# Optimization experiments

Hardware: AMD Instinct MI355X
Metric: run time of the kernel (lower is better)

## Reference

```python
import jax, jax.numpy as jnp
import numpy as np

N_NODES = 10000
AVG_DEG = 16
N_EDGES = N_NODES * AVG_DEG
NODE_DIM, EDGE_DIM, LIN_DIM, HID, OUT, LAYERS = 9, 3, 32, 300, 2, 5


def _init(key, shape, fan_in):
    return jax.random.normal(key, shape, jnp.float32) * (1.0 / np.sqrt(fan_in))


def setup_inputs() -> dict:
    key = jax.random.key(0)
    ks = jax.random.split(key, 18)
    inp = {
        "x": jax.random.normal(ks[0], (N_NODES, NODE_DIM), jnp.float32),
        "edge_index": jax.random.randint(ks[1], (2, N_EDGES), 0, N_NODES, jnp.int32),
        "edge_attr": jax.random.normal(ks[2], (N_EDGES, EDGE_DIM), jnp.float32),
        "batch": jnp.zeros((N_NODES,), jnp.int32),
        # nn.Linear params (stored as [in, out] so fwd is x @ W + b)
        "node_w": _init(ks[3], (NODE_DIM, LIN_DIM), NODE_DIM),
        "node_b": jnp.zeros((LIN_DIM,), jnp.float32),
        "edge_w": _init(ks[4], (EDGE_DIM, LIN_DIM), EDGE_DIM),
        "edge_b": jnp.zeros((LIN_DIM,), jnp.float32),
        # GCNConv: lin (no bias) + separate additive bias (PyG convention)
        "gcn0_w": _init(ks[5], (LIN_DIM, HID), LIN_DIM),
        "gcn0_b": jnp.zeros((HID,), jnp.float32),
        "gcn_w": _init(ks[6], (LAYERS - 1, HID, HID), HID),
        "gcn_b": jnp.zeros((LAYERS - 1, HID), jnp.float32),
        "lin1_w": _init(ks[7], (HID, LIN_DIM), HID),
        "lin1_b": jnp.zeros((LIN_DIM,), jnp.float32),
        "lin2_w": _init(ks[8], (LIN_DIM, OUT), LIN_DIM),
        "lin2_b": jnp.zeros((OUT,), jnp.float32),
    }
    return inp


def reference(x, edge_index, edge_attr, batch,
              node_w, node_b, edge_w, edge_b,
              gcn0_w, gcn0_b, gcn_w, gcn_b,
              lin1_w, lin1_b, lin2_w, lin2_b):
    row, col = edge_index[0], edge_index[1]

    e = edge_attr @ edge_w + edge_b  # [E, LIN_DIM] edge embeddings

    # Faithful to the original bug: node embeddings get edge attrs scatter-added,
    # then the result is discarded by `attr = edge_attr`. Kept for fidelity (dead).
    node_h = x @ node_w + node_b
    node_h = node_h.at[row].add(e)  # unused downstream

    # GCN stack runs over the E-row edge-embedding matrix -> effective node count = E
    h = e
    n = h.shape[0]  # == N_EDGES

    # symmetric gcn_norm with self-loops (edge_weight = 1), computed once
    deg = jax.ops.segment_sum(jnp.ones((edge_index.shape[1],), h.dtype), col,
                              num_segments=n) + 1.0
    dinv = jax.lax.rsqrt(deg)
    norm = dinv[row] * dinv[col]  # per-edge normalization
    self_norm = (dinv * dinv)[:, None]  # self-loop term

    def gcn(h, w, b):
        hw = h @ w  # dense transform
        agg = jax.ops.segment_sum(hw[row] * norm[:, None], col, num_segments=n)
        return agg + self_norm * hw + b

    h = jax.nn.relu(gcn(h, gcn0_w, gcn0_b))

    def step(h, wb):
        w, b = wb
        return jax.nn.relu(gcn(h, w, b)), None

    h, _ = jax.lax.scan(step, h, (gcn_w, gcn_b))

    g = jnp.mean(h, axis=0, keepdims=True)  # [1, HID] graph readout
    g = jax.nn.relu(g @ lin1_w + lin1_b)
    pred = g @ lin2_w + lin2_b  # [1, OUT]; forward returns pre-softmax logits
    return pred
```

## Files before the change

kernel.cpp:

```cpp
#include <hip/hip_runtime.h>
#include <hip/hip_bf16.h>

#define N_NODES 10000
#define N_EDGES 160000
#define HID 300
#define HIDP 304
#define NPARTB (N_EDGES - N_NODES)
#define KS 328
#define RBM 80
#define RBF 16
#define PARTB_BLOCKS 1875
#define GEMMA_BLOCKS 125
#define FILL_BLOCKS 313
#define MEGA_BLOCKS (PARTB_BLOCKS + GEMMA_BLOCKS + FILL_BLOCKS)
#define FUSE_BLOCKS 625

typedef __attribute__((ext_vector_type(8))) short short8;
typedef __attribute__((ext_vector_type(4))) short s16x4;
typedef __attribute__((ext_vector_type(4))) float f32x4;

#define MFMA_B16(a, b, c) __builtin_amdgcn_mfma_f32_16x16x32_bf16(a, b, c, 0, 0, 0)

__device__ __forceinline__ short bf16r(float x) {
    unsigned u = __float_as_uint(x);
    return (short)((u + 0x7fffu + ((u >> 16) & 1u)) >> 16);
}
__device__ __forceinline__ float b2f(unsigned short u) {
    return __uint_as_float(((unsigned)u) << 16);
}
__device__ __forceinline__ void split1(float x, short& hi, short& lo) {
    short h = bf16r(x);
    float hf = __uint_as_float(((unsigned)(unsigned short)h) << 16);
    hi = h;
    lo = bf16r(x - hf);
}

__global__ void k_prep(const float* __restrict__ g0w, const float* __restrict__ gw,
                       short* __restrict__ wt0, short* __restrict__ wtl,
                       const int* __restrict__ col, int* __restrict__ cnt) {
    int idx = blockIdx.x * 256 + threadIdx.x;
    if (idx < N_EDGES) atomicAdd(&cnt[col[idx]], 1);
    if (idx < 1216) {
        int n16 = idx & 15, q = (idx >> 4) & 3, nt = idx >> 6;
        int n = nt * 16 + n16;
        short* hd = wt0 + (size_t)(nt * 8 + q) * 128 + n16 * 8;
        short* ld = wt0 + (size_t)(nt * 8 + 4 + q) * 128 + n16 * 8;
#pragma unroll
        for (int j = 0; j < 8; ++j) {
            int k = q * 8 + j;
            float f = (n < HID) ? g0w[k * HID + n] : 0.0f;
            short hi, lo;
            split1(f, hi, lo);
            hd[j] = hi;
            ld[j] = lo;
        }
    } else if (idx < 1216 + 48640) {
        int i = idx - 1216;
        int n16 = i & 15; i >>= 4;
        int q = i & 3; i >>= 2;
        int nt = i % 19; i /= 19;
        int chunk = i % 10;
        int l = i / 10;
        int n = nt * 16 + n16;
        int cnt_idx = chunk * 19 + nt;
        short* base = wtl + (size_t)l * 194560;
        short* hd = base + (size_t)(cnt_idx * 8 + q) * 128 + n16 * 8;
        short* ld = base + (size_t)(cnt_idx * 8 + 4 + q) * 128 + n16 * 8;
#pragma unroll
        for (int j = 0; j < 8; ++j) {
            int k = chunk * 32 + q * 8 + j;
            float f = (k < HID && n < HID) ? gw[((size_t)l * HID + k) * HID + n] : 0.0f;
            short hi, lo;
            split1(f, hi, lo);
            hd[j] = hi;
            ld[j] = lo;
        }
    }
}

__global__ __launch_bounds__(1024) void k_scan(
    const int* __restrict__ cnt, int* __restrict__ col_start,
    int* __restrict__ cursor, float* __restrict__ dinv,
    float* __restrict__ selfnorm) {
    __shared__ int wsum[16];
    int t = threadIdx.x;
    int lane = t & 63, w = t >> 6;
    int carry = 0;
    for (int base = 0; base < N_NODES; base += 1024) {
        int i = base + t;
        int v = (i < N_NODES) ? cnt[i] : 0;
        int s = v;
#pragma unroll
        for (int d = 1; d < 64; d <<= 1) {
            int n = __shfl_up(s, d, 64);
            if (lane >= d) s += n;
        }
        if (lane == 63) wsum[w] = s;
        __syncthreads();
        int woff = 0, total = 0;
#pragma unroll
        for (int k = 0; k < 16; ++k) {
            if (k < w) woff += wsum[k];
            total += wsum[k];
        }
        if (i < N_NODES) {
            int excl = carry + woff + s - v;
            col_start[i] = excl;
            cursor[i] = excl;
            float dd = (float)v + 1.0f;
            dinv[i] = rsqrtf(dd);
            selfnorm[i] = 1.0f / dd;
        }
        carry += total;
        __syncthreads();
    }
    if (t == 0) col_start[N_NODES] = carry;
}

template <int MT, int NTC>
__device__ __forceinline__ void kloop(const short* __restrict__ wp, int nch,
                                      const short* Hh, int nt0, int quad, int l16,
                                      f32x4 (&acc)[MT][NTC]) {
#pragma unroll
    for (int mt = 0; mt < MT; ++mt)
#pragma unroll
        for (int i = 0; i < NTC; ++i)
#pragma unroll
            for (int r = 0; r < 4; ++r) acc[mt][i][r] = 0.0f;

    const short* a0 = Hh + l16 * KS + quad * 8;
    const short* w0 = wp + (size_t)nt0 * 1024 + (size_t)(quad * 128 + l16 * 8);

    short8 ah[MT], an[MT], b1[NTC], b1n[NTC], b2[NTC];
#pragma unroll
    for (int mt = 0; mt < MT; ++mt) ah[mt] = *(const short8*)(a0 + mt * 16 * KS);
#pragma unroll
    for (int i = 0; i < NTC; ++i) b1[i] = *(const short8*)(w0 + (size_t)i * 1024);

#pragma unroll 1
    for (int c = 0; c < nch - 1; ++c) {
        const short* wc = w0 + (size_t)c * 19456;
        const short* wn = wc + 19456;
        const short* apn = a0 + (c + 1) * 32;
#pragma unroll
        for (int i = 0; i < NTC; ++i) b2[i] = *(const short8*)(wc + (size_t)i * 1024 + 512);
#pragma unroll
        for (int mt = 0; mt < MT; ++mt) an[mt] = *(const short8*)(apn + mt * 16 * KS);
#pragma unroll
        for (int i = 0; i < NTC; ++i) b1n[i] = *(const short8*)(wn + (size_t)i * 1024);
#pragma unroll
        for (int mt = 0; mt < MT; ++mt)
#pragma unroll
            for (int i = 0; i < NTC; ++i) acc[mt][i] = MFMA_B16(ah[mt], b1[i], acc[mt][i]);
#pragma unroll
        for (int mt = 0; mt < MT; ++mt)
#pragma unroll
            for (int i = 0; i < NTC; ++i) acc[mt][i] = MFMA_B16(ah[mt], b2[i], acc[mt][i]);
#pragma unroll
        for (int mt = 0; mt < MT; ++mt) ah[mt] = an[mt];
#pragma unroll
        for (int i = 0; i < NTC; ++i) b1[i] = b1n[i];
    }
    {
        const short* wc = w0 + (size_t)(nch - 1) * 19456;
#pragma unroll
        for (int i = 0; i < NTC; ++i) b2[i] = *(const short8*)(wc + (size_t)i * 1024 + 512);
#pragma unroll
        for (int mt = 0; mt < MT; ++mt)
#pragma unroll
            for (int i = 0; i < NTC; ++i) acc[mt][i] = MFMA_B16(ah[mt], b1[i], acc[mt][i]);
#pragma unroll
        for (int mt = 0; mt < MT; ++mt)
#pragma unroll
            for (int i = 0; i < NTC; ++i) acc[mt][i] = MFMA_B16(ah[mt], b2[i], acc[mt][i]);
    }
}

template <int MT, int NTC>
__device__ __forceinline__ void gcn_epilogue(const float* __restrict__ bias,
                                             int nt0, int quad, int l16,
                                             f32x4 (&acc)[MT][NTC], short* Hh) {
#pragma unroll
    for (int i = 0; i < NTC; ++i) {
        int c = (nt0 + i) * 16 + l16;
        float b = (c < HID) ? bias[c] : 0.0f;
#pragma unroll
        for (int mt = 0; mt < MT; ++mt)
#pragma unroll
            for (int r = 0; r < 4; ++r) {
                float v = fmaxf(acc[mt][i][r] + b, 0.0f);
                Hh[(mt * 16 + quad * 4 + r) * KS + c] = bf16r(v);
            }
    }
}

template <int MT, int NTC>
__device__ __forceinline__ void gcn_final(const float* __restrict__ bias,
                                          int nt0, int quad, int l16,
                                          f32x4 (&acc)[MT][NTC],
                                          float* __restrict__ gout) {
#pragma unroll
    for (int i = 0; i < NTC; ++i) {
        int c = (nt0 + i) * 16 + l16;
        float b = (c < HID) ? bias[c] : 0.0f;
        float s = 0.0f;
#pragma unroll
        for (int mt = 0; mt < MT; ++mt)
#pragma unroll
            for (int r = 0; r < 4; ++r) s += fmaxf(acc[mt][i][r] + b, 0.0f);
        s += __shfl_xor(s, 16, 64);
        s += __shfl_xor(s, 32, 64);
        if (quad == 0) gout[c] = (c < HID) ? s : 0.0f;
    }
}

template <int MT, int NTC>
__device__ __forceinline__ void gemm_out(int base, int nt0, int quad, int l16,
                                         f32x4 (&acc)[MT][NTC],
                                         unsigned short* __restrict__ HW) {
#pragma unroll
    for (int i = 0; i < NTC; ++i) {
        int c = (nt0 + i) * 16 + l16;
#pragma unroll
        for (int mt = 0; mt < MT; ++mt)
#pragma unroll
            for (int r = 0; r < 4; ++r) {
                int gm = base + mt * 16 + quad * 4 + r;
                if (gm < N_NODES)
                    HW[(size_t)gm * HIDP + c] = (unsigned short)bf16r(acc[mt][i][r]);
            }
    }
}

__global__ __launch_bounds__(512, 3) void k_mega(
    const float* __restrict__ edge_attr,
    const float* __restrict__ edge_w,
    const float* __restrict__ edge_b,
    const short* __restrict__ wt0,
    const short* __restrict__ wtl,
    const float* __restrict__ gcn0_b,
    const float* __restrict__ gcn_b,
    float* __restrict__ gpartB,
    unsigned short* __restrict__ hw0,
    const int* __restrict__ row,
    const int* __restrict__ col,
    int* __restrict__ cursor,
    const float* __restrict__ dinv,
    int2* __restrict__ edge_pack) {
    __shared__ short Hh[RBM * KS];
    int bid = blockIdx.x, t = threadIdx.x;
    int lane = t & 63, w = t >> 6;
    int l16 = lane & 15, quad = lane >> 4;
    int nt0 = (w < 3) ? w * 3 : 9 + (w - 3) * 2;

    if (bid < PARTB_BLOCKS) {
        int base = N_NODES + bid * RBM;
        for (int i = t; i < RBM * 8; i += 512) {
            int r = i >> 3, c4 = (i & 7) * 4;
            const float* ar = edge_attr + (size_t)(base + r) * 3;
            float a0 = ar[0], a1 = ar[1], a2 = ar[2];
#pragma unroll
            for (int j = 0; j < 4; ++j) {
                int cc = c4 + j;
                float v = edge_b[cc];
                v = fmaf(a0, edge_w[cc], v);
                v = fmaf(a1, edge_w[32 + cc], v);
                v = fmaf(a2, edge_w[64 + cc], v);
                Hh[r * KS + cc] = bf16r(v);
            }
        }
        for (int i = t; i < RBM * 24; i += 512) {
            int r = i / 24, k = 304 + i % 24;
            Hh[r * KS + k] = 0;
        }
        __syncthreads();

        float* gout = gpartB + (size_t)bid * HIDP;
        if (w < 3) {
            f32x4 acc[5][3];
            kloop<5, 3>(wt0, 1, Hh, nt0, quad, l16, acc);
            __syncthreads();
            gcn_epilogue<5, 3>(gcn0_b, nt0, quad, l16, acc, Hh);
            __syncthreads();
            for (int l = 0; l < 4; ++l) {
                kloop<5, 3>(wtl + (size_t)l * 194560, 10, Hh, nt0, quad, l16, acc);
                __syncthreads();
                if (l < 3) {
                    gcn_epilogue<5, 3>(gcn_b + l * HID, nt0, quad, l16, acc, Hh);
                    __syncthreads();
                } else {
                    gcn_final<5, 3>(gcn_b + l * HID, nt0, quad, l16, acc, gout);
                }
            }
        } else {
            f32x4 acc[5][2];
            kloop<5, 2>(wt0, 1, Hh, nt0, quad, l16, acc);
            __syncthreads();
            gcn_epilogue<5, 2>(gcn0_b, nt0, quad, l16, acc, Hh);
            __syncthreads();
            for (int l = 0; l < 4; ++l) {
                kloop<5, 2>(wtl + (size_t)l * 194560, 10, Hh, nt0, quad, l16, acc);
                __syncthreads();
                if (l < 3) {
                    gcn_epilogue<5, 2>(gcn_b + l * HID, nt0, quad, l16, acc, Hh);
                    __syncthreads();
                } else {
                    gcn_final<5, 2>(gcn_b + l * HID, nt0, quad, l16, acc, gout);
                }
            }
        }
    } else if (bid < PARTB_BLOCKS + GEMMA_BLOCKS) {
        int base = (bid - PARTB_BLOCKS) * RBM;
        for (int i = t; i < RBM * 8; i += 512) {
            int r = i >> 3, c4 = (i & 7) * 4;
            const float* ar = edge_attr + (size_t)(base + r) * 3;
            float a0 = ar[0], a1 = ar[1], a2 = ar[2];
#pragma unroll
            for (int j = 0; j < 4; ++j) {
                int cc = c4 + j;
                float v = edge_b[cc];
                v = fmaf(a0, edge_w[cc], v);
                v = fmaf(a1, edge_w[32 + cc], v);
                v = fmaf(a2, edge_w[64 + cc], v);
                Hh[r * KS + cc] = bf16r(v);
            }
        }
        for (int i = t; i < RBM * 24; i += 512) {
            int r = i / 24, k = 304 + i % 24;
            Hh[r * KS + k] = 0;
        }
        __syncthreads();
        if (w < 3) {
            f32x4 acc[5][3];
            kloop<5, 3>(wt0, 1, Hh, nt0, quad, l16, acc);
            gemm_out<5, 3>(base, nt0, quad, l16, acc, hw0);
        } else {
            f32x4 acc[5][2];
            kloop<5, 2>(wt0, 1, Hh, nt0, quad, l16, acc);
            gemm_out<5, 2>(base, nt0, quad, l16, acc, hw0);
        }
    } else {
        int e = (bid - PARTB_BLOCKS - GEMMA_BLOCKS) * 512 + t;
        if (e < N_EDGES) {
            int c = col[e], r = row[e];
            int p = atomicAdd(&cursor[c], 1);
            edge_pack[p] = make_int2(r, __float_as_int(dinv[r] * dinv[c]));
        }
    }
}

__device__ __forceinline__ void agg_row(int c, int lane,
                                        const unsigned short* __restrict__ hw_in,
                                        const int* __restrict__ col_start,
                                        const int2* __restrict__ edge_pack,
                                        float (&v)[5]) {
#pragma unroll
    for (int jj = 0; jj < 5; ++jj) v[jj] = 0.0f;
    int beg = col_start[c], end = col_start[c + 1];
    int i = beg;
#pragma unroll 1
    for (; i + 8 <= end; i += 8) {
        int2 e0 = edge_pack[i], e1 = edge_pack[i + 1];
        int2 e2 = edge_pack[i + 2], e3 = edge_pack[i + 3];
        int2 e4 = edge_pack[i + 4], e5 = edge_pack[i + 5];
        int2 e6 = edge_pack[i + 6], e7 = edge_pack[i + 7];
        const unsigned short* h0 = hw_in + (size_t)e0.x * HIDP;
        const unsigned short* h1 = hw_in + (size_t)e1.x * HIDP;
        const unsigned short* h2 = hw_in + (size_t)e2.x * HIDP;
        const unsigned short* h3 = hw_in + (size_t)e3.x * HIDP;
        const unsigned short* h4 = hw_in + (size_t)e4.x * HIDP;
        const unsigned short* h5 = hw_in + (size_t)e5.x * HIDP;
        const unsigned short* h6 = hw_in + (size_t)e6.x * HIDP;
        const unsigned short* h7 = hw_in + (size_t)e7.x * HIDP;
        float n0 = __int_as_float(e0.y), n1 = __int_as_float(e1.y);
        float n2 = __int_as_float(e2.y), n3 = __int_as_float(e3.y);
        float n4 = __int_as_float(e4.y), n5 = __int_as_float(e5.y);
        float n6 = __int_as_float(e6.y), n7 = __int_as_float(e7.y);
#pragma unroll
        for (int jj = 0; jj < 5; ++jj) {
            int cc = lane + 64 * jj;
            if (cc < HIDP) {
                float s = v[jj];
                s = fmaf(n0, b2f(h0[cc]), s);
                s = fmaf(n1, b2f(h1[cc]), s);
                s = fmaf(n2, b2f(h2[cc]), s);
                s = fmaf(n3, b2f(h3[cc]), s);
                s = fmaf(n4, b2f(h4[cc]), s);
                s = fmaf(n5, b2f(h5[cc]), s);
                s = fmaf(n6, b2f(h6[cc]), s);
                s = fmaf(n7, b2f(h7[cc]), s);
                v[jj] = s;
            }
        }
    }
#pragma unroll 1
    for (; i + 4 <= end; i += 4) {
        int2 e0 = edge_pack[i], e1 = edge_pack[i + 1];
        int2 e2 = edge_pack[i + 2], e3 = edge_pack[i + 3];
        const unsigned short* h0 = hw_in + (size_t)e0.x * HIDP;
        const unsigned short* h1 = hw_in + (size_t)e1.x * HIDP;
        const unsigned short* h2 = hw_in + (size_t)e2.x * HIDP;
        const unsigned short* h3 = hw_in + (size_t)e3.x * HIDP;
        float n0 = __int_as_float(e0.y), n1 = __int_as_float(e1.y);
        float n2 = __int_as_float(e2.y), n3 = __int_as_float(e3.y);
#pragma unroll
        for (int jj = 0; jj < 5; ++jj) {
            int cc = lane + 64 * jj;
            if (cc < HIDP) {
                float s = v[jj];
                s = fmaf(n0, b2f(h0[cc]), s);
                s = fmaf(n1, b2f(h1[cc]), s);
                s = fmaf(n2, b2f(h2[cc]), s);
                s = fmaf(n3, b2f(h3[cc]), s);
                v[jj] = s;
            }
        }
    }
#pragma unroll 1
    for (; i < end; ++i) {
        int2 e0 = edge_pack[i];
        const unsigned short* h0 = hw_in + (size_t)e0.x * HIDP;
        float n0 = __int_as_float(e0.y);
#pragma unroll
        for (int jj = 0; jj < 5; ++jj) {
            int cc = lane + 64 * jj;
            if (cc < HIDP) v[jj] = fmaf(n0, b2f(h0[cc]), v[jj]);
        }
    }
}

__global__ __launch_bounds__(512, 4) void k_fuse(
    const unsigned short* __restrict__ hw_in,
    const int* __restrict__ col_start,
    const int2* __restrict__ edge_pack,
    const float* __restrict__ selfnorm,
    const float* __restrict__ bias,
    const short* __restrict__ wt,
    unsigned short* __restrict__ hw_out) {
    __shared__ short Hh[RBF * KS];
    int t = threadIdx.x;
    int lane = t & 63, w = t >> 6;
    int l16 = lane & 15, quad = lane >> 4;
    int base = blockIdx.x * RBF;
    int nt0 = (w < 3) ? w * 3 : 9 + (w - 3) * 2;

#pragma unroll 1
    for (int j = 0; j < 2; ++j) {
        int r = w * 2 + j;
        int c = base + r;
        float v[5];
        agg_row(c, lane, hw_in, col_start, edge_pack, v);
        float sn = selfnorm[c];
        const unsigned short* sp = hw_in + (size_t)c * HIDP;
#pragma unroll
        for (int jj = 0; jj < 5; ++jj) {
            int cc = lane + 64 * jj;
            if (cc < HIDP) {
                float h = v[jj] + sn * b2f(sp[cc]) + ((cc < HID) ? bias[cc] : 0.0f);
                Hh[r * KS + cc] = bf16r(fmaxf(h, 0.0f));
            }
        }
    }
    for (int i = t; i < RBF * 6; i += 512) {
        int r = i / 6, k = 304 + (i % 6) * 4;
        *(s16x4*)&Hh[r * KS + k] = (s16x4)0;
    }
    __syncthreads();

    if (w < 3) {
        f32x4 acc[1][3];
        kloop<1, 3>(wt, 10, Hh, nt0, quad, l16, acc);
        gemm_out<1, 3>(base, nt0, quad, l16, acc, hw_out);
    } else {
        f32x4 acc[1][2];
        kloop<1, 2>(wt, 10, Hh, nt0, quad, l16, acc);
        gemm_out<1, 2>(base, nt0, quad, l16, acc, hw_out);
    }
}

__global__ __launch_bounds__(512) void k_last(
    const unsigned short* __restrict__ hw_in,
    const int* __restrict__ col_start,
    const int2* __restrict__ edge_pack,
    const float* __restrict__ selfnorm,
    const float* __restrict__ bias,
    const float* __restrict__ gpartB,
    float* __restrict__ g_sum) {
    __shared__ float red[8 * 320];
    int t = threadIdx.x;
    int lane = t & 63, w = t >> 6;
    int base = blockIdx.x * RBF;

    float s[5] = {0.0f, 0.0f, 0.0f, 0.0f, 0.0f};
#pragma unroll 1
    for (int j = 0; j < 2; ++j) {
        int c = base + w * 2 + j;
        float v[5];
        agg_row(c, lane, hw_in, col_start, edge_pack, v);
        float sn = selfnorm[c];
        const unsigned short* sp = hw_in + (size_t)c * HIDP;
#pragma unroll
        for (int jj = 0; jj < 5; ++jj) {
            int cc = lane + 64 * jj;
            if (cc < HID) {
                float h = v[jj] + sn * b2f(sp[cc]) + bias[cc];
                s[jj] += fmaxf(h, 0.0f);
            }
        }
    }
    if (w < 3) {
        int rr = blockIdx.x * 3 + w;
        if (rr < PARTB_BLOCKS) {
#pragma unroll
            for (int jj = 0; jj < 5; ++jj) {
                int cc = lane + 64 * jj;
                if (cc < HID) s[jj] += gpartB[(size_t)rr * HIDP + cc];
            }
        }
    }
#pragma unroll
    for (int jj = 0; jj < 5; ++jj) red[w * 320 + lane + 64 * jj] = s[jj];
    __syncthreads();
    if (w == 0) {
#pragma unroll
        for (int jj = 0; jj < 5; ++jj) {
            int cc = lane + 64 * jj;
            if (cc < HID) {
                float tot = 0.0f;
#pragma unroll
                for (int g = 0; g < 8; ++g) tot += red[g * 320 + cc];
                atomicAdd(&g_sum[cc], tot);
            }
        }
    }
}

__global__ void k_head(const float* __restrict__ g_sum,
                       const float* __restrict__ lin1_w, const float* __restrict__ lin1_b,
                       const float* __restrict__ lin2_w, const float* __restrict__ lin2_b,
                       float* __restrict__ out) {
    __shared__ float g2[32];
    int t = threadIdx.x;
    const float inv = 1.0f / (float)N_EDGES;
    if (t < 32) {
        float a = lin1_b[t];
        for (int d = 0; d < HID; ++d) a = fmaf(g_sum[d] * inv, lin1_w[d * 32 + t], a);
        g2[t] = fmaxf(a, 0.0f);
    }
    __syncthreads();
    if (t < 2) {
        float p = lin2_b[t];
        for (int j = 0; j < 32; ++j) p = fmaf(g2[j], lin2_w[j * 2 + t], p);
        out[t] = p;
    }
}


extern "C" void kernel_launch(void* const* d_in, const int* in_sizes, int n_in,
                              void* d_out, int out_size, void* d_ws, size_t ws_size,
                              hipStream_t stream) {
    (void)in_sizes; (void)n_in; (void)out_size; (void)ws_size;
    const int* edge_index = (const int*)d_in[1];
    const float* edge_attr = (const float*)d_in[2];
    const float* edge_w = (const float*)d_in[6];
    const float* edge_b = (const float*)d_in[7];
    const float* gcn0_w = (const float*)d_in[8];
    const float* gcn0_b = (const float*)d_in[9];
    const float* gcn_w = (const float*)d_in[10];
    const float* gcn_b = (const float*)d_in[11];
    const float* lin1_w = (const float*)d_in[12];
    const float* lin1_b = (const float*)d_in[13];
    const float* lin2_w = (const float*)d_in[14];
    const float* lin2_b = (const float*)d_in[15];

    char* ws = (char*)d_ws;
    size_t off = 0;
    auto alloc = [&](size_t bytes) {
        void* p = ws + off;
        off = (off + bytes + 255) & ~(size_t)255;
        return p;
    };
    unsigned short* hwA = (unsigned short*)alloc((size_t)N_NODES * HIDP * 2);
    unsigned short* hwB = (unsigned short*)alloc((size_t)N_NODES * HIDP * 2);
    int2* edge_pack = (int2*)alloc((size_t)N_EDGES * 8);
    int* cnt = (int*)alloc((size_t)N_NODES * 4);
    int* col_start = (int*)alloc((size_t)(N_NODES + 1) * 4);
    int* cursor = (int*)alloc((size_t)N_NODES * 4);
    float* dinv = (float*)alloc((size_t)N_NODES * 4);
    float* selfnorm = (float*)alloc((size_t)N_NODES * 4);
    float* g_sum = (float*)alloc((size_t)HIDP * 4);
    short* wt0 = (short*)alloc((size_t)38912);
    short* wtl = (short*)alloc((size_t)4 * 389120);
    float* gpartB = (float*)alloc((size_t)PARTB_BLOCKS * HIDP * 4);

    const int* row = edge_index;
    const int* col = edge_index + N_EDGES;

    hipMemsetAsync(cnt, 0, N_NODES * 4, stream);
    hipMemsetAsync(g_sum, 0, HIDP * 4, stream);

    k_prep<<<(N_EDGES + 255) / 256, 256, 0, stream>>>(gcn0_w, gcn_w, wt0, wtl, col, cnt);
    k_scan<<<1, 1024, 0, stream>>>(cnt, col_start, cursor, dinv, selfnorm);

    k_mega<<<MEGA_BLOCKS, 512, 0, stream>>>(edge_attr, edge_w, edge_b, wt0, wtl,
                                            gcn0_b, gcn_b, gpartB, hwA,
                                            row, col, cursor, dinv, edge_pack);

    k_fuse<<<FUSE_BLOCKS, 512, 0, stream>>>(hwA, col_start, edge_pack, selfnorm,
                                            gcn0_b, wtl + (size_t)0 * 194560, hwB);
    k_fuse<<<FUSE_BLOCKS, 512, 0, stream>>>(hwB, col_start, edge_pack, selfnorm,
                                            gcn_b + 0 * HID, wtl + (size_t)1 * 194560, hwA);
    k_fuse<<<FUSE_BLOCKS, 512, 0, stream>>>(hwA, col_start, edge_pack, selfnorm,
                                            gcn_b + 1 * HID, wtl + (size_t)2 * 194560, hwB);
    k_fuse<<<FUSE_BLOCKS, 512, 0, stream>>>(hwB, col_start, edge_pack, selfnorm,
                                            gcn_b + 2 * HID, wtl + (size_t)3 * 194560, hwA);
    k_last<<<FUSE_BLOCKS, 512, 0, stream>>>(hwA, col_start, edge_pack, selfnorm,
                                            gcn_b + 3 * HID, gpartB, g_sum);
    k_head<<<1, 64, 0, stream>>>(g_sum, lin1_w, lin1_b, lin2_w, lin2_b, (float*)d_out);
}
```

Baseline: 492.9 us.

## Vectorize aggregation gathers to 4-wide bf16 loads and simplify GEMM k-loop

The edge aggregation in the fused and last-layer kernels now has each lane gather 4 contiguous bf16 values per neighbor row with 8-byte loads, two chunks per lane, instead of 5 scalar 2-byte loads. This is meant to cut the number of memory instructions in the gather-bound aggregation. The MFMA k-loop drops its software-pipelined register prefetch for a simpler load-then-compute loop, which may expose more load latency but uses fewer registers. The mega kernel's launch bound rises to 4 waves per EU, trading registers for occupancy.

```diff
diff --git a/kernel.cpp b/kernel.cpp
--- a/kernel.cpp
+++ b/kernel.cpp
@@ -28,6 +28,12 @@
 __device__ __forceinline__ float b2f(unsigned short u) {
     return __uint_as_float(((unsigned)u) << 16);
 }
+__device__ __forceinline__ float blo(unsigned u) {
+    return __uint_as_float(u << 16);
+}
+__device__ __forceinline__ float bhi(unsigned u) {
+    return __uint_as_float(u & 0xffff0000u);
+}
 __device__ __forceinline__ void split1(float x, short& hi, short& lo) {
     short h = bf16r(x);
     float hf = __uint_as_float(((unsigned)(unsigned short)h) << 16);
@@ -127,52 +133,28 @@
         for (int i = 0; i < NTC; ++i)
 #pragma unroll
             for (int r = 0; r < 4; ++r) acc[mt][i][r] = 0.0f;
-
-    const short* a0 = Hh + l16 * KS + quad * 8;
-    const short* w0 = wp + (size_t)nt0 * 1024 + (size_t)(quad * 128 + l16 * 8);
-
-    short8 ah[MT], an[MT], b1[NTC], b1n[NTC], b2[NTC];
-#pragma unroll
-    for (int mt = 0; mt < MT; ++mt) ah[mt] = *(const short8*)(a0 + mt * 16 * KS);
-#pragma unroll
-    for (int i = 0; i < NTC; ++i) b1[i] = *(const short8*)(w0 + (size_t)i * 1024);
-
 #pragma unroll 1
-    for (int c = 0; c < nch - 1; ++c) {
-        const short* wc = w0 + (size_t)c * 19456;
-        const short* wn = wc + 19456;
-        const short* apn = a0 + (c + 1) * 32;
-#pragma unroll
-        for (int i = 0; i < NTC; ++i) b2[i] = *(const short8*)(wc + (size_t)i * 1024 + 512);
-#pragma unroll
-        for (int mt = 0; mt < MT; ++mt) an[mt] = *(const short8*)(apn + mt * 16 * KS);
-#pragma unroll
-        for (int i = 0; i < NTC; ++i) b1n[i] = *(const short8*)(wn + (size_t)i * 1024);
+    for (int c = 0; c < nch; ++c) {
+        const short* cb = wp + (size_t)(c * 19 + nt0) * 1024 + quad * 128 + l16 * 8;
+        short8 ah[MT];
 #pragma unroll
         for (int mt = 0; mt < MT; ++mt)
-#pragma unroll
-            for (int i = 0; i < NTC; ++i) acc[mt][i] = MFMA_B16(ah[mt], b1[i], acc[mt][i]);
+            ah[mt] = *(const short8*)&Hh[(mt * 16 + l16) * KS + c * 32 + quad * 8];
+        short8 bb[NTC];
+#pragma unroll
+        for (int i = 0; i < NTC; ++i) bb[i] = *(const short8*)(cb + (size_t)i * 1024);
 #pragma unroll
         for (int mt = 0; mt < MT; ++mt)
 #pragma unroll
-            for (int i = 0; i < NTC; ++i) acc[mt][i] = MFMA_B16(ah[mt], b2[i], acc[mt][i]);
-#pragma unroll
-        for (int mt = 0; mt < MT; ++mt) ah[mt] = an[mt];
-#pragma unroll
-        for (int i = 0; i < NTC; ++i) b1[i] = b1n[i];
-    }
-    {
-        const short* wc = w0 + (size_t)(nch - 1) * 19456;
-#pragma unroll
-        for (int i = 0; i < NTC; ++i) b2[i] = *(const short8*)(wc + (size_t)i * 1024 + 512);
+            for (int i = 0; i < NTC; ++i)
+                acc[mt][i] = MFMA_B16(ah[mt], bb[i], acc[mt][i]);
+#pragma unroll
+        for (int i = 0; i < NTC; ++i) bb[i] = *(const short8*)(cb + (size_t)i * 1024 + 512);
 #pragma unroll
         for (int mt = 0; mt < MT; ++mt)
 #pragma unroll
-            for (int i = 0; i < NTC; ++i) acc[mt][i] = MFMA_B16(ah[mt], b1[i], acc[mt][i]);
-#pragma unroll
-        for (int mt = 0; mt < MT; ++mt)
-#pragma unroll
-            for (int i = 0; i < NTC; ++i) acc[mt][i] = MFMA_B16(ah[mt], b2[i], acc[mt][i]);
+            for (int i = 0; i < NTC; ++i)
+                acc[mt][i] = MFMA_B16(ah[mt], bb[i], acc[mt][i]);
     }
 }
 
@@ -232,7 +214,7 @@
     }
 }
 
-__global__ __launch_bounds__(512, 3) void k_mega(
+__global__ __launch_bounds__(512, 4) void k_mega(
     const float* __restrict__ edge_attr,
     const float* __restrict__ edge_w,
     const float* __restrict__ edge_b,
@@ -349,14 +331,23 @@
     }
 }
 
-__device__ __forceinline__ void agg_row(int c, int lane,
-                                        const unsigned short* __restrict__ hw_in,
-                                        const int* __restrict__ col_start,
-                                        const int2* __restrict__ edge_pack,
-                                        float (&v)[5]) {
-#pragma unroll
-    for (int jj = 0; jj < 5; ++jj) v[jj] = 0.0f;
+__device__ __forceinline__ void fma4(float (&v)[4], float n, uint2 q) {
+    v[0] = fmaf(n, blo(q.x), v[0]);
+    v[1] = fmaf(n, bhi(q.x), v[1]);
+    v[2] = fmaf(n, blo(q.y), v[2]);
+    v[3] = fmaf(n, bhi(q.y), v[3]);
+}
+
+__device__ __forceinline__ void agg_row4(int c, int lane,
+                                         const unsigned short* __restrict__ hw_in,
+                                         const int* __restrict__ col_start,
+                                         const int2* __restrict__ edge_pack,
+                                         float (&v0)[4], float (&v1)[4]) {
+#pragma unroll
+    for (int k = 0; k < 4; ++k) { v0[k] = 0.0f; v1[k] = 0.0f; }
     int beg = col_start[c], end = col_start[c + 1];
+    int cb0 = 4 * lane;
+    int cb1 = 256 + 4 * lane;
     int i = beg;
 #pragma unroll 1
     for (; i + 8 <= end; i += 8) {
@@ -372,26 +363,26 @@
         const unsigned short* h5 = hw_in + (size_t)e5.x * HIDP;
         const unsigned short* h6 = hw_in + (size_t)e6.x * HIDP;
         const unsigned short* h7 = hw_in + (size_t)e7.x * HIDP;
+        uint2 a0 = *(const uint2*)(h0 + cb0), b0 = *(const uint2*)(h0 + cb1);
+        uint2 a1 = *(const uint2*)(h1 + cb0), b1 = *(const uint2*)(h1 + cb1);
+        uint2 a2 = *(const uint2*)(h2 + cb0), b2 = *(const uint2*)(h2 + cb1);
+        uint2 a3 = *(const uint2*)(h3 + cb0), b3 = *(const uint2*)(h3 + cb1);
+        uint2 a4 = *(const uint2*)(h4 + cb0), b4 = *(const uint2*)(h4 + cb1);
+        uint2 a5 = *(const uint2*)(h5 + cb0), b5 = *(const uint2*)(h5 + cb1);
+        uint2 a6 = *(const uint2*)(h6 + cb0), b6 = *(const uint2*)(h6 + cb1);
+        uint2 a7 = *(const uint2*)(h7 + cb0), b7 = *(const uint2*)(h7 + cb1);
         float n0 = __int_as_float(e0.y), n1 = __int_as_float(e1.y);
         float n2 = __int_as_float(e2.y), n3 = __int_as_float(e3.y);
         float n4 = __int_as_float(e4.y), n5 = __int_as_float(e5.y);
         float n6 = __int_as_float(e6.y), n7 = __int_as_float(e7.y);
-#pragma unroll
-        for (int jj = 0; jj < 5; ++jj) {
-            int cc = lane + 64 * jj;
-            if (cc < HIDP) {
-                float s = v[jj];
-                s = fmaf(n0, b2f(h0[cc]), s);
-                s = fmaf(n1, b2f(h1[cc]), s);
-                s = fmaf(n2, b2f(h2[cc]), s);
-                s = fmaf(n3, b2f(h3[cc]), s);
-                s = fmaf(n4, b2f(h4[cc]), s);
-                s = fmaf(n5, b2f(h5[cc]), s);
-                s = fmaf(n6, b2f(h6[cc]), s);
-                s = fmaf(n7, b2f(h7[cc]), s);
-                v[jj] = s;
-            }
-        }
+        fma4(v0, n0, a0); fma4(v1, n0, b0);
+        fma4(v0, n1, a1); fma4(v1, n1, b1);
+        fma4(v0, n2, a2); fma4(v1, n2, b2);
+        fma4(v0, n3, a3); fma4(v1, n3, b3);
+        fma4(v0, n4, a4); fma4(v1, n4, b4);
+        fma4(v0, n5, a5); fma4(v1, n5, b5);
+        fma4(v0, n6, a6); fma4(v1, n6, b6);
+        fma4(v0, n7, a7); fma4(v1, n7, b7);
     }
 #pragma unroll 1
     for (; i + 4 <= end; i += 4) {
@@ -401,31 +392,24 @@
         const unsigned short* h1 = hw_in + (size_t)e1.x * HIDP;
         const unsigned short* h2 = hw_in + (size_t)e2.x * HIDP;
         const unsigned short* h3 = hw_in + (size_t)e3.x * HIDP;
+        uint2 a0 = *(const uint2*)(h0 + cb0), b0 = *(const uint2*)(h0 + cb1);
+        uint2 a1 = *(const uint2*)(h1 + cb0), b1 = *(const uint2*)(h1 + cb1);
+        uint2 a2 = *(const uint2*)(h2 + cb0), b2 = *(const uint2*)(h2 + cb1);
+        uint2 a3 = *(const uint2*)(h3 + cb0), b3 = *(const uint2*)(h3 + cb1);
         float n0 = __int_as_float(e0.y), n1 = __int_as_float(e1.y);
         float n2 = __int_as_float(e2.y), n3 = __int_as_float(e3.y);
-#pragma unroll
-        for (int jj = 0; jj < 5; ++jj) {
-            int cc = lane + 64 * jj;
-            if (cc < HIDP) {
-                float s = v[jj];
-                s = fmaf(n0, b2f(h0[cc]), s);
-                s = fmaf(n1, b2f(h1[cc]), s);
-                s = fmaf(n2, b2f(h2[cc]), s);
-                s = fmaf(n3, b2f(h3[cc]), s);
-                v[jj] = s;
-            }
-        }
+        fma4(v0, n0, a0); fma4(v1, n0, b0);
+        fma4(v0, n1, a1); fma4(v1, n1, b1);
+        fma4(v0, n2, a2); fma4(v1, n2, b2);
+        fma4(v0, n3, a3); fma4(v1, n3, b3);
     }
 #pragma unroll 1
     for (; i < end; ++i) {
         int2 e0 = edge_pack[i];
         const unsigned short* h0 = hw_in + (size_t)e0.x * HIDP;
+        uint2 a0 = *(const uint2*)(h0 + cb0), b0 = *(const uint2*)(h0 + cb1);
         float n0 = __int_as_float(e0.y);
-#pragma unroll
-        for (int jj = 0; jj < 5; ++jj) {
-            int cc = lane + 64 * jj;
-            if (cc < HIDP) v[jj] = fmaf(n0, b2f(h0[cc]), v[jj]);
-        }
+        fma4(v0, n0, a0); fma4(v1, n0, b0);
     }
 }
 
@@ -443,22 +427,35 @@
     int l16 = lane & 15, quad = lane >> 4;
     int base = blockIdx.x * RBF;
     int nt0 = (w < 3) ? w * 3 : 9 + (w - 3) * 2;
+    int cb0 = 4 * lane, cb1 = 256 + 4 * lane;
 
 #pragma unroll 1
     for (int j = 0; j < 2; ++j) {
         int r = w * 2 + j;
         int c = base + r;
-        float v[5];
-        agg_row(c, lane, hw_in, col_start, edge_pack, v);
+        float v0[4], v1[4];
+        agg_row4(c, lane, hw_in, col_start, edge_pack, v0, v1);
         float sn = selfnorm[c];
         const unsigned short* sp = hw_in + (size_t)c * HIDP;
-#pragma unroll
-        for (int jj = 0; jj < 5; ++jj) {
-            int cc = lane + 64 * jj;
-            if (cc < HIDP) {
-                float h = v[jj] + sn * b2f(sp[cc]) + ((cc < HID) ? bias[cc] : 0.0f);
-                Hh[r * KS + cc] = bf16r(fmaxf(h, 0.0f));
-            }
+        uint2 s0 = *(const uint2*)(sp + cb0);
+        float4 bv = *(const float4*)(bias + cb0);
+        s16x4 pk;
+        pk[0] = bf16r(fmaxf(v0[0] + sn * blo(s0.x) + bv.x, 0.0f));
+        pk[1] = bf16r(fmaxf(v0[1] + sn * bhi(s0.x) + bv.y, 0.0f));
+        pk[2] = bf16r(fmaxf(v0[2] + sn * blo(s0.y) + bv.z, 0.0f));
+        pk[3] = bf16r(fmaxf(v0[3] + sn * bhi(s0.y) + bv.w, 0.0f));
+        *(s16x4*)&Hh[r * KS + cb0] = pk;
+        if (lane < 12) {
+            uint2 s1 = *(const uint2*)(sp + cb1);
+            float sv[4] = {sn * blo(s1.x), sn * bhi(s1.x), sn * blo(s1.y), sn * bhi(s1.y)};
+            s16x4 pk2;
+#pragma unroll
+            for (int k = 0; k < 4; ++k) {
+                int cc = cb1 + k;
+                float b = (cc < HID) ? bias[cc] : 0.0f;
+                pk2[k] = bf16r(fmaxf(v1[k] + sv[k] + b, 0.0f));
+            }
+            *(s16x4*)&Hh[r * KS + cb1] = pk2;
         }
     }
     for (int i = t; i < RBF * 6; i += 512) {
@@ -490,46 +487,70 @@
     int t = threadIdx.x;
     int lane = t & 63, w = t >> 6;
     int base = blockIdx.x * RBF;
-
-    float s[5] = {0.0f, 0.0f, 0.0f, 0.0f, 0.0f};
+    int cb0 = 4 * lane, cb1 = 256 + 4 * lane;
+
+    float s0[4] = {0.0f, 0.0f, 0.0f, 0.0f};
+    float s1[4] = {0.0f, 0.0f, 0.0f, 0.0f};
 #pragma unroll 1
     for (int j = 0; j < 2; ++j) {
         int c = base + w * 2 + j;
-        float v[5];
-        agg_row(c, lane, hw_in, col_start, edge_pack, v);
+        float v0[4], v1[4];
+        agg_row4(c, lane, hw_in, col_start, edge_pack, v0, v1);
         float sn = selfnorm[c];
         const unsigned short* sp = hw_in + (size_t)c * HIDP;
-#pragma unroll
-        for (int jj = 0; jj < 5; ++jj) {
-            int cc = lane + 64 * jj;
-            if (cc < HID) {
-                float h = v[jj] + sn * b2f(sp[cc]) + bias[cc];
-                s[jj] += fmaxf(h, 0.0f);
+        uint2 q0 = *(const uint2*)(sp + cb0);
+        float4 bv = *(const float4*)(bias + cb0);
+        s0[0] += fmaxf(v0[0] + sn * blo(q0.x) + bv.x, 0.0f);
+        s0[1] += fmaxf(v0[1] + sn * bhi(q0.x) + bv.y, 0.0f);
+        s0[2] += fmaxf(v0[2] + sn * blo(q0.y) + bv.z, 0.0f);
+        s0[3] += fmaxf(v0[3] + sn * bhi(q0.y) + bv.w, 0.0f);
+        if (lane < 12) {
+            uint2 q1 = *(const uint2*)(sp + cb1);
+            float sv[4] = {sn * blo(q1.x), sn * bhi(q1.x), sn * blo(q1.y), sn * bhi(q1.y)};
+#pragma unroll
+            for (int k = 0; k < 4; ++k) {
+                int cc = cb1 + k;
+                if (cc < HID) s1[k] += fmaxf(v1[k] + sv[k] + bias[cc], 0.0f);
             }
         }
     }
     if (w < 3) {
         int rr = blockIdx.x * 3 + w;
         if (rr < PARTB_BLOCKS) {
-#pragma unroll
-            for (int jj = 0; jj < 5; ++jj) {
-                int cc = lane + 64 * jj;
-                if (cc < HID) s[jj] += gpartB[(size_t)rr * HIDP + cc];
-            }
-        }
-    }
-#pragma unroll
-    for (int jj = 0; jj < 5; ++jj) red[w * 320 + lane + 64 * jj] = s[jj];
+            const float* gp = gpartB + (size_t)rr * HIDP;
+            float4 g0 = *(const float4*)(gp + cb0);
+            s0[0] += g0.x; s0[1] += g0.y; s0[2] += g0.z; s0[3] += g0.w;
+            if (lane < 12) {
+#pragma unroll
+                for (int k = 0; k < 4; ++k) {
+                    int cc = cb1 + k;
+                    if (cc < HID) s1[k] += gp[cc];
+                }
+            }
+        }
+    }
+    *(float4*)&red[w * 320 + cb0] = make_float4(s0[0], s0[1], s0[2], s0[3]);
+    if (lane < 12) *(float4*)&red[w * 320 + cb1] = make_float4(s1[0], s1[1], s1[2], s1[3]);
     __syncthreads();
     if (w == 0) {
 #pragma unroll
-        for (int jj = 0; jj < 5; ++jj) {
-            int cc = lane + 64 * jj;
-            if (cc < HID) {
-                float tot = 0.0f;
-#pragma unroll
-                for (int g = 0; g < 8; ++g) tot += red[g * 320 + cc];
-                atomicAdd(&g_sum[cc], tot);
+        for (int k = 0; k < 4; ++k) {
+            int cc = cb0 + k;
+            float tot = 0.0f;
+#pragma unroll
+            for (int g = 0; g < 8; ++g) tot += red[g * 320 + cc];
+            atomicAdd(&g_sum[cc], tot);
+        }
+        if (lane < 12) {
+#pragma unroll
+            for (int k = 0; k < 4; ++k) {
+                int cc = cb1 + k;
+                if (cc < HID) {
+                    float tot = 0.0f;
+#pragma unroll
+                    for (int g = 0; g < 8; ++g) tot += red[g * 320 + cc];
+                    atomicAdd(&g_sum[cc], tot);
+                }
             }
         }
     }
```

Result: slower. 526.6 us (+6.8%).

## Interleave two-row aggregation in fuse/last kernels and simplify mega GEMM loop

Applied to the files above, without the earlier changes.

Replaces the per-row sequential neighbor aggregation with a paired routine that gathers four edges for each of two destination rows at once, raising memory-level parallelism in the gather. The old software-pipelined k-loop is renamed kloop_p and used by k_fuse, while a simpler non-pipelined kloop is now used by k_mega. k_mega's launch bounds change from 3 to 4 waves per SIMD to raise occupancy. The simpler loop and tighter register budget may lose latency hiding or cause spills in the GEMM phase.

```diff
diff --git a/kernel.cpp b/kernel.cpp
--- a/kernel.cpp
+++ b/kernel.cpp
@@ -127,6 +127,41 @@
         for (int i = 0; i < NTC; ++i)
 #pragma unroll
             for (int r = 0; r < 4; ++r) acc[mt][i][r] = 0.0f;
+#pragma unroll 1
+    for (int c = 0; c < nch; ++c) {
+        const short* cb = wp + (size_t)(c * 19 + nt0) * 1024 + quad * 128 + l16 * 8;
+        short8 ah[MT];
+#pragma unroll
+        for (int mt = 0; mt < MT; ++mt)
+            ah[mt] = *(const short8*)&Hh[(mt * 16 + l16) * KS + c * 32 + quad * 8];
+        short8 bb[NTC];
+#pragma unroll
+        for (int i = 0; i < NTC; ++i) bb[i] = *(const short8*)(cb + (size_t)i * 1024);
+#pragma unroll
+        for (int mt = 0; mt < MT; ++mt)
+#pragma unroll
+            for (int i = 0; i < NTC; ++i)
+                acc[mt][i] = MFMA_B16(ah[mt], bb[i], acc[mt][i]);
+#pragma unroll
+        for (int i = 0; i < NTC; ++i) bb[i] = *(const short8*)(cb + (size_t)i * 1024 + 512);
+#pragma unroll
+        for (int mt = 0; mt < MT; ++mt)
+#pragma unroll
+            for (int i = 0; i < NTC; ++i)
+                acc[mt][i] = MFMA_B16(ah[mt], bb[i], acc[mt][i]);
+    }
+}
+
+template <int MT, int NTC>
+__device__ __forceinline__ void kloop_p(const short* __restrict__ wp, int nch,
+                                        const short* Hh, int nt0, int quad, int l16,
+                                        f32x4 (&acc)[MT][NTC]) {
+#pragma unroll
+    for (int mt = 0; mt < MT; ++mt)
+#pragma unroll
+        for (int i = 0; i < NTC; ++i)
+#pragma unroll
+            for (int r = 0; r < 4; ++r) acc[mt][i][r] = 0.0f;
 
     const short* a0 = Hh + l16 * KS + quad * 8;
     const short* w0 = wp + (size_t)nt0 * 1024 + (size_t)(quad * 128 + l16 * 8);
@@ -232,7 +267,7 @@
     }
 }
 
-__global__ __launch_bounds__(512, 3) void k_mega(
+__global__ __launch_bounds__(512, 4) void k_mega(
     const float* __restrict__ edge_attr,
     const float* __restrict__ edge_w,
     const float* __restrict__ edge_b,
@@ -349,82 +384,100 @@
     }
 }
 
-__device__ __forceinline__ void agg_row(int c, int lane,
-                                        const unsigned short* __restrict__ hw_in,
-                                        const int* __restrict__ col_start,
-                                        const int2* __restrict__ edge_pack,
-                                        float (&v)[5]) {
-#pragma unroll
-    for (int jj = 0; jj < 5; ++jj) v[jj] = 0.0f;
-    int beg = col_start[c], end = col_start[c + 1];
-    int i = beg;
+__device__ __forceinline__ void agg_edge4(int i, int lane, int cap,
+                                          const unsigned short* __restrict__ hw_in,
+                                          const int2* __restrict__ ep,
+                                          float (&v)[5]) {
+    int2 e0 = ep[i], e1 = ep[i + 1], e2 = ep[i + 2], e3 = ep[i + 3];
+    const unsigned short* h0 = hw_in + (size_t)e0.x * HIDP;
+    const unsigned short* h1 = hw_in + (size_t)e1.x * HIDP;
+    const unsigned short* h2 = hw_in + (size_t)e2.x * HIDP;
+    const unsigned short* h3 = hw_in + (size_t)e3.x * HIDP;
+    float n0 = __int_as_float(e0.y), n1 = __int_as_float(e1.y);
+    float n2 = __int_as_float(e2.y), n3 = __int_as_float(e3.y);
+#pragma unroll
+    for (int jj = 0; jj < 5; ++jj) {
+        int cc = lane + 64 * jj;
+        if (cc < cap) {
+            float s = v[jj];
+            s = fmaf(n0, b2f(h0[cc]), s);
+            s = fmaf(n1, b2f(h1[cc]), s);
+            s = fmaf(n2, b2f(h2[cc]), s);
+            s = fmaf(n3, b2f(h3[cc]), s);
+            v[jj] = s;
+        }
+    }
+}
+
+__device__ __forceinline__ void agg_pair(int c0, int c1, int lane,
+                                         const unsigned short* __restrict__ hw_in,
+                                         const int* __restrict__ col_start,
+                                         const int2* __restrict__ ep,
+                                         float (&v0)[5], float (&v1)[5]) {
+#pragma unroll
+    for (int jj = 0; jj < 5; ++jj) { v0[jj] = 0.0f; v1[jj] = 0.0f; }
+    int i0 = col_start[c0], e0 = col_start[c0 + 1];
+    int i1 = col_start[c1], e1 = col_start[c1 + 1];
 #pragma unroll 1
-    for (; i + 8 <= end; i += 8) {
-        int2 e0 = edge_pack[i], e1 = edge_pack[i + 1];
-        int2 e2 = edge_pack[i + 2], e3 = edge_pack[i + 3];
-        int2 e4 = edge_pack[i + 4], e5 = edge_pack[i + 5];
-        int2 e6 = edge_pack[i + 6], e7 = edge_pack[i + 7];
-        const unsigned short* h0 = hw_in + (size_t)e0.x * HIDP;
-        const unsigned short* h1 = hw_in + (size_t)e1.x * HIDP;
-        const unsigned short* h2 = hw_in + (size_t)e2.x * HIDP;
-        const unsigned short* h3 = hw_in + (size_t)e3.x * HIDP;
-        const unsigned short* h4 = hw_in + (size_t)e4.x * HIDP;
-        const unsigned short* h5 = hw_in + (size_t)e5.x * HIDP;
-        const unsigned short* h6 = hw_in + (size_t)e6.x * HIDP;
-        const unsigned short* h7 = hw_in + (size_t)e7.x * HIDP;
-        float n0 = __int_as_float(e0.y), n1 = __int_as_float(e1.y);
-        float n2 = __int_as_float(e2.y), n3 = __int_as_float(e3.y);
-        float n4 = __int_as_float(e4.y), n5 = __int_as_float(e5.y);
-        float n6 = __int_as_float(e6.y), n7 = __int_as_float(e7.y);
+    while (i0 + 4 <= e0 && i1 + 4 <= e1) {
+        int2 a0 = ep[i0], a1 = ep[i0 + 1], a2 = ep[i0 + 2], a3 = ep[i0 + 3];
+        int2 b0 = ep[i1], b1 = ep[i1 + 1], b2 = ep[i1 + 2], b3 = ep[i1 + 3];
+        const unsigned short* pa0 = hw_in + (size_t)a0.x * HIDP;
+        const unsigned short* pa1 = hw_in + (size_t)a1.x * HIDP;
+        const unsigned short* pa2 = hw_in + (size_t)a2.x * HIDP;
+        const unsigned short* pa3 = hw_in + (size_t)a3.x * HIDP;
+        const unsigned short* pb0 = hw_in + (size_t)b0.x * HIDP;
+        const unsigned short* pb1 = hw_in + (size_t)b1.x * HIDP;
+        const unsigned short* pb2 = hw_in + (size_t)b2.x * HIDP;
+        const unsigned short* pb3 = hw_in + (size_t)b3.x * HIDP;
+        float na0 = __int_as_float(a0.y), na1 = __int_as_float(a1.y);
+        float na2 = __int_as_float(a2.y), na3 = __int_as_float(a3.y);
+        float nb0 = __int_as_float(b0.y), nb1 = __int_as_float(b1.y);
+        float nb2 = __int_as_float(b2.y), nb3 = __int_as_float(b3.y);
 #pragma unroll
         for (int jj = 0; jj < 5; ++jj) {
             int cc = lane + 64 * jj;
             if (cc < HIDP) {
-                float s = v[jj];
-                s = fmaf(n0, b2f(h0[cc]), s);
-                s = fmaf(n1, b2f(h1[cc]), s);
-                s = fmaf(n2, b2f(h2[cc]), s);
-                s = fmaf(n3, b2f(h3[cc]), s);
-                s = fmaf(n4, b2f(h4[cc]), s);
-                s = fmaf(n5, b2f(h5[cc]), s);
-                s = fmaf(n6, b2f(h6[cc]), s);
-                s = fmaf(n7, b2f(h7[cc]), s);
-                v[jj] = s;
-            }
-        }
+                float s = v0[jj];
+                s = fmaf(na0, b2f(pa0[cc]), s);
+                s = fmaf(na1, b2f(pa1[cc]), s);
+                s = fmaf(na2, b2f(pa2[cc]), s);
+                s = fmaf(na3, b2f(pa3[cc]), s);
+                v0[jj] = s;
+                float u = v1[jj];
+                u = fmaf(nb0, b2f(pb0[cc]), u);
+                u = fmaf(nb1, b2f(pb1[cc]), u);
+                u = fmaf(nb2, b2f(pb2[cc]), u);
+                u = fmaf(nb3, b2f(pb3[cc]), u);
+                v1[jj] = u;
+            }
+        }
+        i0 += 4; i1 += 4;
     }
 #pragma unroll 1
-    for (; i + 4 <= end; i += 4) {
-        int2 e0 = edge_pack[i], e1 = edge_pack[i + 1];
-        int2 e2 = edge_pack[i + 2], e3 = edge_pack[i + 3];
-        const unsigned short* h0 = hw_in + (size_t)e0.x * HIDP;
-        const unsigned short* h1 = hw_in + (size_t)e1.x * HIDP;
-        const unsigned short* h2 = hw_in + (size_t)e2.x * HIDP;
-        const unsigned short* h3 = hw_in + (size_t)e3.x * HIDP;
-        float n0 = __int_as_float(e0.y), n1 = __int_as_float(e1.y);
-        float n2 = __int_as_float(e2.y), n3 = __int_as_float(e3.y);
+    for (; i0 + 4 <= e0; i0 += 4) agg_edge4(i0, lane, HIDP, hw_in, ep, v0);
+#pragma unroll 1
+    for (; i0 < e0; ++i0) {
+        int2 q = ep[i0];
+        const unsigned short* h = hw_in + (size_t)q.x * HIDP;
+        float n = __int_as_float(q.y);
 #pragma unroll
         for (int jj = 0; jj < 5; ++jj) {
             int cc = lane + 64 * jj;
-            if (cc < HIDP) {
-                float s = v[jj];
-                s = fmaf(n0, b2f(h0[cc]), s);
-                s = fmaf(n1, b2f(h1[cc]), s);
-                s = fmaf(n2, b2f(h2[cc]), s);
-                s = fmaf(n3, b2f(h3[cc]), s);
-                v[jj] = s;
-            }
+            if (cc < HIDP) v0[jj] = fmaf(n, b2f(h[cc]), v0[jj]);
         }
     }
 #pragma unroll 1
-    for (; i < end; ++i) {
-        int2 e0 = edge_pack[i];
-        const unsigned short* h0 = hw_in + (size_t)e0.x * HIDP;
-        float n0 = __int_as_float(e0.y);
+    for (; i1 + 4 <= e1; i1 += 4) agg_edge4(i1, lane, HIDP, hw_in, ep, v1);
+#pragma unroll 1
+    for (; i1 < e1; ++i1) {
+        int2 q = ep[i1];
+        const unsigned short* h = hw_in + (size_t)q.x * HIDP;
+        float n = __int_as_float(q.y);
 #pragma unroll
         for (int jj = 0; jj < 5; ++jj) {
             int cc = lane + 64 * jj;
-            if (cc < HIDP) v[jj] = fmaf(n0, b2f(h0[cc]), v[jj]);
+            if (cc < HIDP) v1[jj] = fmaf(n, b2f(h[cc]), v1[jj]);
         }
     }
 }
@@ -444,20 +497,23 @@
     int base = blockIdx.x * RBF;
     int nt0 = (w < 3) ? w * 3 : 9 + (w - 3) * 2;
 
-#pragma unroll 1
-    for (int j = 0; j < 2; ++j) {
-        int r = w * 2 + j;
-        int c = base + r;
-        float v[5];
-        agg_row(c, lane, hw_in, col_start, edge_pack, v);
-        float sn = selfnorm[c];
-        const unsigned short* sp = hw_in + (size_t)c * HIDP;
+    {
+        int c0 = base + w * 2, c1 = c0 + 1;
+        float v0[5], v1[5];
+        agg_pair(c0, c1, lane, hw_in, col_start, edge_pack, v0, v1);
+        float sn0 = selfnorm[c0], sn1 = selfnorm[c1];
+        const unsigned short* sp0 = hw_in + (size_t)c0 * HIDP;
+        const unsigned short* sp1 = hw_in + (size_t)c1 * HIDP;
+        int r0 = w * 2;
 #pragma unroll
         for (int jj = 0; jj < 5; ++jj) {
             int cc = lane + 64 * jj;
             if (cc < HIDP) {
-                float h = v[jj] + sn * b2f(sp[cc]) + ((cc < HID) ? bias[cc] : 0.0f);
-                Hh[r * KS + cc] = bf16r(fmaxf(h, 0.0f));
+                float b = (cc < HID) ? bias[cc] : 0.0f;
+                float h0 = v0[jj] + sn0 * b2f(sp0[cc]) + b;
+                float h1 = v1[jj] + sn1 * b2f(sp1[cc]) + b;
+                Hh[r0 * KS + cc] = bf16r(fmaxf(h0, 0.0f));
+                Hh[(r0 + 1) * KS + cc] = bf16r(fmaxf(h1, 0.0f));
             }
         }
     }
@@ -469,11 +525,11 @@
 
     if (w < 3) {
         f32x4 acc[1][3];
-        kloop<1, 3>(wt, 10, Hh, nt0, quad, l16, acc);
+        kloop_p<1, 3>(wt, 10, Hh, nt0, quad, l16, acc);
         gemm_out<1, 3>(base, nt0, quad, l16, acc, hw_out);
     } else {
         f32x4 acc[1][2];
-        kloop<1, 2>(wt, 10, Hh, nt0, quad, l16, acc);
+        kloop_p<1, 2>(wt, 10, Hh, nt0, quad, l16, acc);
         gemm_out<1, 2>(base, nt0, quad, l16, acc, hw_out);
     }
 }
@@ -492,19 +548,20 @@
     int base = blockIdx.x * RBF;
 
     float s[5] = {0.0f, 0.0f, 0.0f, 0.0f, 0.0f};
-#pragma unroll 1
-    for (int j = 0; j < 2; ++j) {
-        int c = base + w * 2 + j;
-        float v[5];
-        agg_row(c, lane, hw_in, col_start, edge_pack, v);
-        float sn = selfnorm[c];
-        const unsigned short* sp = hw_in + (size_t)c * HIDP;
+    {
+        int c0 = base + w * 2, c1 = c0 + 1;
+        float v0[5], v1[5];
+        agg_pair(c0, c1, lane, hw_in, col_start, edge_pack, v0, v1);
+        float sn0 = selfnorm[c0], sn1 = selfnorm[c1];
+        const unsigned short* sp0 = hw_in + (size_t)c0 * HIDP;
+        const unsigned short* sp1 = hw_in + (size_t)c1 * HIDP;
 #pragma unroll
         for (int jj = 0; jj < 5; ++jj) {
             int cc = lane + 64 * jj;
             if (cc < HID) {
-                float h = v[jj] + sn * b2f(sp[cc]) + bias[cc];
-                s[jj] += fmaxf(h, 0.0f);
+                float b = bias[cc];
+                s[jj] += fmaxf(v0[jj] + sn0 * b2f(sp0[cc]) + b, 0.0f);
+                s[jj] += fmaxf(v1[jj] + sn1 * b2f(sp1[cc]) + b, 0.0f);
             }
         }
     }
```

Measured after the change: 460.1 us. 6.6% less time.
